# Optimization experiments

Hardware: AMD Instinct MI355X
Metric: run time of the kernel (lower is better)

The kernel has to match this reference:

```python
import jax, jax.numpy as jnp
import numpy as np

N_ENT = 500000
N_REL = 1000
EMB = 256
B = 65536
EPS = 1e-12


def setup_inputs() -> dict:
    key = jax.random.key(0)
    ks = jax.random.split(key, 7)
    all_emb = jax.random.normal(ks[0], (N_ENT + N_REL, EMB), dtype=jnp.float32)
    pos_h = jax.random.randint(ks[1], (B,), 0, N_ENT)
    pos_r = jax.random.randint(ks[2], (B,), 0, N_REL)
    pos_t = jax.random.randint(ks[3], (B,), 0, N_ENT)
    neg_h = jax.random.randint(ks[4], (B,), 0, N_ENT)
    neg_r = jax.random.randint(ks[5], (B,), 0, N_REL)
    neg_t = jax.random.randint(ks[6], (B,), 0, N_ENT)
    return {"all_emb": all_emb, "pos_h": pos_h, "pos_r": pos_r, "pos_t": pos_t,
            "neg_h": neg_h, "neg_r": neg_r, "neg_t": neg_t, "n_ent": N_ENT}


def reference(all_emb, pos_h, pos_r, pos_t, neg_h, neg_r, neg_t, n_ent):
    # forward() first L2-normalizes entity rows in-place (normalize_entity_weights)
    ent = all_emb[:n_ent]
    nrm = jnp.maximum(jnp.linalg.norm(ent, axis=1, keepdims=True), EPS)
    emb = jnp.concatenate([ent / nrm, all_emb[n_ent:]], axis=0)

    # sparse.mm(adj, emb) with rows (+1@h, +1@(n_ent+r), -1@t) == gather-combine
    def score(h, r, t):
        v = emb[h] + emb[r + n_ent] - emb[t]          # [B, EMB]
        return -jnp.sum(v * v, axis=1)                 # -||.||_2^2, [B]

    pos_calc = score(pos_h, pos_r, pos_t)
    neg_calc = score(neg_h, neg_r, neg_t)
    return (pos_calc, neg_calc)
```

## Files before the change

kernel.cpp:

```cpp
#include <hip/hip_runtime.h>


#define EMB 256
#define EPS 1e-12f
#define SPW 4

__global__ __launch_bounds__(256) void transe_score_kernel(
    const float* __restrict__ emb,
    const int* __restrict__ pos_h, const int* __restrict__ pos_r, const int* __restrict__ pos_t,
    const int* __restrict__ neg_h, const int* __restrict__ neg_r, const int* __restrict__ neg_t,
    const int* __restrict__ n_ent_ptr,
    float* __restrict__ out, int B)
{
    const int wave = (blockIdx.x * blockDim.x + threadIdx.x) >> 6;
    const int lane = threadIdx.x & 63;
    const int base = wave * SPW;
    if (base >= 2 * B) return;

    const int n_ent = *n_ent_ptr;

    const int* __restrict__ hsrc;
    const int* __restrict__ rsrc;
    const int* __restrict__ tsrc;
    int off;
    if (base < B) { hsrc = pos_h; rsrc = pos_r; tsrc = pos_t; off = base; }
    else          { hsrc = neg_h; rsrc = neg_r; tsrc = neg_t; off = base - B; }

    const int4 hh = *(const int4*)(hsrc + off);
    const int4 rr = *(const int4*)(rsrc + off);
    const int4 tt = *(const int4*)(tsrc + off);

    const int hi[SPW] = {hh.x, hh.y, hh.z, hh.w};
    const int ri[SPW] = {rr.x, rr.y, rr.z, rr.w};
    const int ti[SPW] = {tt.x, tt.y, tt.z, tt.w};

    float4 hv[SPW], tv[SPW], rv[SPW];
#pragma unroll
    for (int s = 0; s < SPW; ++s) {
        hv[s] = ((const float4*)(emb + (size_t)hi[s] * EMB))[lane];
        tv[s] = ((const float4*)(emb + (size_t)ti[s] * EMB))[lane];
        rv[s] = ((const float4*)(emb + ((size_t)ri[s] + (size_t)n_ent) * EMB))[lane];
    }

    float red[2 * SPW];
#pragma unroll
    for (int s = 0; s < SPW; ++s) {
        red[s]       = hv[s].x * hv[s].x + hv[s].y * hv[s].y + hv[s].z * hv[s].z + hv[s].w * hv[s].w;
        red[SPW + s] = tv[s].x * tv[s].x + tv[s].y * tv[s].y + tv[s].z * tv[s].z + tv[s].w * tv[s].w;
    }
#pragma unroll
    for (int d = 32; d >= 1; d >>= 1) {
#pragma unroll
        for (int k = 0; k < 2 * SPW; ++k)
            red[k] += __shfl_xor(red[k], d, 64);
    }

    float sq[SPW];
#pragma unroll
    for (int s = 0; s < SPW; ++s) {
        const float inh = 1.0f / fmaxf(sqrtf(red[s]), EPS);
        const float itn = 1.0f / fmaxf(sqrtf(red[SPW + s]), EPS);
        const float vx = hv[s].x * inh + rv[s].x - tv[s].x * itn;
        const float vy = hv[s].y * inh + rv[s].y - tv[s].y * itn;
        const float vz = hv[s].z * inh + rv[s].z - tv[s].z * itn;
        const float vw = hv[s].w * inh + rv[s].w - tv[s].w * itn;
        sq[s] = vx * vx + vy * vy + vz * vz + vw * vw;
    }
#pragma unroll
    for (int d = 32; d >= 1; d >>= 1) {
#pragma unroll
        for (int k = 0; k < SPW; ++k)
            sq[k] += __shfl_xor(sq[k], d, 64);
    }

    if (lane == 0)
        *(float4*)(out + base) = make_float4(-sq[0], -sq[1], -sq[2], -sq[3]);
}

extern "C" void kernel_launch(void* const* d_in, const int* in_sizes, int n_in,
                              void* d_out, int out_size, void* d_ws, size_t ws_size,
                              hipStream_t stream) {
    const float* emb  = (const float*)d_in[0];
    const int* pos_h  = (const int*)d_in[1];
    const int* pos_r  = (const int*)d_in[2];
    const int* pos_t  = (const int*)d_in[3];
    const int* neg_h  = (const int*)d_in[4];
    const int* neg_r  = (const int*)d_in[5];
    const int* neg_t  = (const int*)d_in[6];
    const int* n_ent  = (const int*)d_in[7];
    float* out = (float*)d_out;

    const int B = in_sizes[1];
    const int total = 2 * B;
    const int waves = (total + SPW - 1) / SPW;
    const int block = 256;
    const int grid = (waves * 64 + block - 1) / block;

    transe_score_kernel<<<grid, block, 0, stream>>>(
        emb, pos_h, pos_r, pos_t, neg_h, neg_r, neg_t, n_ent, out, B);
}
```

Measured before the change: 604.8 us.

## Precompute entity inverse norms and stage gathered rows through LDS

```diff
diff --git a/kernel.cpp b/kernel.cpp
--- a/kernel.cpp
+++ b/kernel.cpp
@@ -3,9 +3,128 @@
 
 #define EMB 256
 #define EPS 1e-12f
+
+#define NRM_RPW 4
+
+__global__ __launch_bounds__(256) void inv_norm_kernel(
+    const float* __restrict__ emb, float* __restrict__ inv_norm,
+    const int* __restrict__ n_ent_ptr)
+{
+    const int wave = (blockIdx.x * blockDim.x + threadIdx.x) >> 6;
+    const int lane = threadIdx.x & 63;
+    const int n_ent = *n_ent_ptr;
+    const int base = wave * NRM_RPW;
+    if (base >= n_ent) return;
+
+    float s[NRM_RPW];
+#pragma unroll
+    for (int i = 0; i < NRM_RPW; ++i) {
+        const int row = base + i;
+        float4 v = make_float4(0.f, 0.f, 0.f, 0.f);
+        if (row < n_ent)
+            v = ((const float4*)(emb + (size_t)row * EMB))[lane];
+        s[i] = v.x * v.x + v.y * v.y + v.z * v.z + v.w * v.w;
+    }
+#pragma unroll
+    for (int d = 32; d >= 1; d >>= 1)
+#pragma unroll
+        for (int i = 0; i < NRM_RPW; ++i)
+            s[i] += __shfl_xor(s[i], d, 64);
+
+    if (lane == 0) {
+        const float4 o = make_float4(
+            1.0f / fmaxf(sqrtf(s[0]), EPS),
+            1.0f / fmaxf(sqrtf(s[1]), EPS),
+            1.0f / fmaxf(sqrtf(s[2]), EPS),
+            1.0f / fmaxf(sqrtf(s[3]), EPS));
+        if (base + NRM_RPW <= n_ent) {
+            *(float4*)(inv_norm + base) = o;
+        } else {
+            inv_norm[base] = o.x;
+            if (base + 1 < n_ent) inv_norm[base + 1] = o.y;
+            if (base + 2 < n_ent) inv_norm[base + 2] = o.z;
+        }
+    }
+}
+
 #define SPW 4
-
-__global__ __launch_bounds__(256) void transe_score_kernel(
+#define WPB 4
+
+__global__ __launch_bounds__(256, 5) void transe_score_lds_kernel(
+    const float* __restrict__ emb,
+    const float* __restrict__ inv_norm,
+    const int* __restrict__ pos_h, const int* __restrict__ pos_r, const int* __restrict__ pos_t,
+    const int* __restrict__ neg_h, const int* __restrict__ neg_r, const int* __restrict__ neg_t,
+    const int* __restrict__ n_ent_ptr,
+    float* __restrict__ out, int B)
+{
+    __shared__ float lds[WPB * 2 * SPW * EMB];
+
+    const int wave = (blockIdx.x * blockDim.x + threadIdx.x) >> 6;
+    const int lane = threadIdx.x & 63;
+    const int wib  = threadIdx.x >> 6;
+    const int base = wave * SPW;
+    if (base >= 2 * B) return;
+
+    const int n_ent = *n_ent_ptr;
+
+    const int* __restrict__ hsrc;
+    const int* __restrict__ rsrc;
+    const int* __restrict__ tsrc;
+    int off;
+    if (base < B) { hsrc = pos_h; rsrc = pos_r; tsrc = pos_t; off = base; }
+    else          { hsrc = neg_h; rsrc = neg_r; tsrc = neg_t; off = base - B; }
+
+    const int4 hh = *(const int4*)(hsrc + off);
+    const int4 rr = *(const int4*)(rsrc + off);
+    const int4 tt = *(const int4*)(tsrc + off);
+    const int hi[SPW] = {hh.x, hh.y, hh.z, hh.w};
+    const int ri[SPW] = {rr.x, rr.y, rr.z, rr.w};
+    const int ti[SPW] = {tt.x, tt.y, tt.z, tt.w};
+
+    float* wl = lds + wib * (2 * SPW * EMB);
+#pragma unroll
+    for (int s = 0; s < SPW; ++s) {
+        const float* hg = emb + (size_t)hi[s] * EMB + lane * 4;
+        const float* tg = emb + (size_t)ti[s] * EMB + lane * 4;
+        __builtin_amdgcn_global_load_lds(hg, wl + s * EMB,         16, 0, 0);
+        __builtin_amdgcn_global_load_lds(tg, wl + (SPW + s) * EMB, 16, 0, 0);
+    }
+
+    float4 rv[SPW];
+    float inh[SPW], itn[SPW];
+#pragma unroll
+    for (int s = 0; s < SPW; ++s) {
+        rv[s]  = ((const float4*)(emb + ((size_t)ri[s] + (size_t)n_ent) * EMB))[lane];
+        inh[s] = inv_norm[hi[s]];
+        itn[s] = inv_norm[ti[s]];
+    }
+
+    asm volatile("s_waitcnt vmcnt(0)" ::: "memory");
+    __builtin_amdgcn_sched_barrier(0);
+
+    float sq[SPW];
+#pragma unroll
+    for (int s = 0; s < SPW; ++s) {
+        const float4 hv = ((const float4*)(wl + s * EMB))[lane];
+        const float4 tv = ((const float4*)(wl + (SPW + s) * EMB))[lane];
+        const float vx = hv.x * inh[s] + rv[s].x - tv.x * itn[s];
+        const float vy = hv.y * inh[s] + rv[s].y - tv.y * itn[s];
+        const float vz = hv.z * inh[s] + rv[s].z - tv.z * itn[s];
+        const float vw = hv.w * inh[s] + rv[s].w - tv.w * itn[s];
+        sq[s] = vx * vx + vy * vy + vz * vz + vw * vw;
+    }
+#pragma unroll
+    for (int d = 32; d >= 1; d >>= 1)
+#pragma unroll
+        for (int k = 0; k < SPW; ++k)
+            sq[k] += __shfl_xor(sq[k], d, 64);
+
+    if (lane == 0)
+        *(float4*)(out + base) = make_float4(-sq[0], -sq[1], -sq[2], -sq[3]);
+}
+
+__global__ __launch_bounds__(256) void transe_score_fused_kernel(
     const float* __restrict__ emb,
     const int* __restrict__ pos_h, const int* __restrict__ pos_r, const int* __restrict__ pos_t,
     const int* __restrict__ neg_h, const int* __restrict__ neg_r, const int* __restrict__ neg_t,
@@ -92,10 +211,22 @@
 
     const int B = in_sizes[1];
     const int total = 2 * B;
-    const int waves = (total + SPW - 1) / SPW;
-    const int block = 256;
-    const int grid = (waves * 64 + block - 1) / block;
-
-    transe_score_kernel<<<grid, block, 0, stream>>>(
-        emb, pos_h, pos_r, pos_t, neg_h, neg_r, neg_t, n_ent, out, B);
-}
+    const size_t rows_total = (size_t)in_sizes[0] / EMB;
+
+    const int waves_b = (total + SPW - 1) / SPW;
+    const int grid_b  = (waves_b * 64 + 255) / 256;
+
+    if (d_ws != nullptr && ws_size >= rows_total * sizeof(float)) {
+        float* inv_norm = (float*)d_ws;
+
+        const long long waves_a = ((long long)rows_total + NRM_RPW - 1) / NRM_RPW;
+        const int grid_a = (int)((waves_a * 64 + 255) / 256);
+
+        inv_norm_kernel<<<grid_a, 256, 0, stream>>>(emb, inv_norm, n_ent);
+        transe_score_lds_kernel<<<grid_b, 256, 0, stream>>>(
+            emb, inv_norm, pos_h, pos_r, pos_t, neg_h, neg_r, neg_t, n_ent, out, B);
+    } else {
+        transe_score_fused_kernel<<<grid_b, 256, 0, stream>>>(
+            emb, pos_h, pos_r, pos_t, neg_h, neg_r, neg_t, n_ent, out, B);
+    }
+}
```

New measurement: 695.8 us. 15.1% more time.
